# Optimization experiments

Measured on AMD Instinct MI355X. Metric: run time of the kernel, lower is better.

Reference implementation:

```python
import jax, jax.numpy as jnp
import numpy as np

N_NODES, N_EDGES, D_IN, D_HID, D_OUT = 100000, 3200000, 128, 64, 10


def _gcn_norm(src, dst, n):
    # symmetric normalization deg^{-1/2}[src] * deg^{-1/2}[dst]; edge weights = 1
    ones = jnp.ones(src.shape[0], jnp.float32)
    deg = jax.ops.segment_sum(ones, dst, num_segments=n)
    dinv = jnp.where(deg > 0, jax.lax.rsqrt(jnp.maximum(deg, 1.0)), 0.0)
    return dinv[src] * dinv[dst]


def _gcn_conv(x, W, b, src, dst, norm, n):
    h = x @ W                                   # [N, out]
    msg = norm[:, None] * jnp.take(h, src, axis=0)  # [E+N, out]
    return jax.ops.segment_sum(msg, dst, num_segments=n) + b


def setup_inputs() -> dict:
    key = jax.random.key(0)
    ks = jax.random.split(key, 8)
    x = jax.random.normal(ks[0], (N_NODES, D_IN), jnp.float32)
    edge_index = jax.random.randint(ks[1], (2, N_EDGES), 0, N_NODES, jnp.int32)
    def glorot(k, fan_in, fan_out):
        s = (6.0 / (fan_in + fan_out)) ** 0.5
        return jax.random.uniform(k, (fan_in, fan_out), jnp.float32, -s, s)
    return {
        "x": x,
        "edge_index": edge_index,
        "W1": glorot(ks[2], D_IN, D_HID), "b1": jnp.zeros((D_HID,), jnp.float32),
        "W2": glorot(ks[3], D_HID, D_HID), "b2": jnp.zeros((D_HID,), jnp.float32),
        "W3": glorot(ks[4], D_HID, D_OUT), "b3": jnp.zeros((D_OUT,), jnp.float32),
    }


def reference(x, edge_index, W1, b1, W2, b2, W3, b3):
    n = x.shape[0]
    loops = jnp.arange(n, dtype=edge_index.dtype)
    src = jnp.concatenate([edge_index[0], loops])  # add self-loops (PyG default)
    dst = jnp.concatenate([edge_index[1], loops])
    norm = _gcn_norm(src, dst, n)                  # identical for all 3 layers
    h = jax.nn.relu(_gcn_conv(x, W1, b1, src, dst, norm, n))
    h = jax.nn.relu(_gcn_conv(h, W2, b2, src, dst, norm, n))
    return _gcn_conv(h, W3, b3, src, dst, norm, n)
```

## Files before the change

### kernel.cpp

```cpp
#include <hip/hip_runtime.h>


constexpr int BK_SHIFT = 6;
constexpr int BK_NODES = 64;
constexpr int BK_CAP   = 2432;
constexpr int MAXNB    = 1568;

__device__ __forceinline__ unsigned short f2bf(float f) {
    unsigned u = __builtin_bit_cast(unsigned, f);
    u += 0x7FFF + ((u >> 16) & 1);
    return (unsigned short)(u >> 16);
}
__device__ __forceinline__ float bf_lo(unsigned d) {
    return __builtin_bit_cast(float, d << 16);
}
__device__ __forceinline__ float bf_hi(unsigned d) {
    return __builtin_bit_cast(float, d & 0xFFFF0000u);
}

__global__ void k_cursor_init(int* __restrict__ cursor, int nb) {
    int i = blockIdx.x * blockDim.x + threadIdx.x;
    if (i < nb) cursor[i] = i * BK_CAP;
}

__global__ void k_partition(const int* __restrict__ src, const int* __restrict__ dst,
                            int E, int nb, int* __restrict__ cursor,
                            unsigned* __restrict__ inter) {
    __shared__ int lcount[MAXNB];
    __shared__ int gbase[MAXNB];
    int t = threadIdx.x;
    int base = blockIdx.x * 16384;
    for (int i = t; i < MAXNB; i += 512) lcount[i] = 0;
    __syncthreads();
    int sv[32], dvv[32];
#pragma unroll
    for (int j = 0; j < 32; j++) {
        int idx = base + j * 512 + t;
        if (idx < E) {
            sv[j] = src[idx]; dvv[j] = dst[idx];
            atomicAdd(&lcount[dvv[j] >> BK_SHIFT], 1);
        } else dvv[j] = -1;
    }
    __syncthreads();
    for (int i = t; i < nb; i += 512) {
        int c = lcount[i]; int g = 0;
        if (c) g = atomicAdd(&cursor[i], c);
        gbase[i] = g; lcount[i] = 0;
    }
    __syncthreads();
#pragma unroll
    for (int j = 0; j < 32; j++) {
        if (dvv[j] >= 0) {
            int b = dvv[j] >> BK_SHIFT;
            int r = atomicAdd(&lcount[b], 1);
            int pos = gbase[b] + r;
            if (pos < (b + 1) * BK_CAP)
                inter[pos] = (unsigned)sv[j] | ((unsigned)(dvv[j] & (BK_NODES - 1)) << 20);
        }
    }
}

__global__ void k_dinvb(const unsigned* __restrict__ inter, const int* __restrict__ cursor,
                        float* __restrict__ dinv, int N) {
    __shared__ int hist[BK_NODES];
    int t = threadIdx.x, b = blockIdx.x;
    if (t < BK_NODES) hist[t] = 0;
    __syncthreads();
    int start = b * BK_CAP;
    int cnt = min(cursor[b] - start, BK_CAP);
    for (int i = t; i < cnt; i += 256) atomicAdd(&hist[inter[start + i] >> 20], 1);
    __syncthreads();
    if (t < BK_NODES) {
        int d = b * BK_NODES + t;
        if (d < N) dinv[d] = rsqrtf((float)(hist[t] + 1));
    }
}

template <int K>
__global__ void k_gemm64bf(const float* __restrict__ X, const float* __restrict__ W,
                           const float* __restrict__ dinv,
                           unsigned short* __restrict__ Y, int n) {
    __shared__ float ws[K * 64];
    __shared__ float xs[16 * K];
    int t = threadIdx.x;
    for (int i = t; i < K * 64; i += 256) ws[i] = W[i];
    int nb = blockIdx.x * 16;
    for (int i = t; i < 16 * K; i += 256) {
        int r = i / K, c = i % K;
        int node = nb + r;
        xs[i] = (node < n) ? X[(size_t)node * K + c] : 0.f;
    }
    __syncthreads();
    int node = t >> 4;
    int ch0  = (t & 15) * 4;
    float ax = 0.f, ay = 0.f, az = 0.f, aw = 0.f;
    for (int k = 0; k < K; k++) {
        float xv = xs[node * K + k];
        const float4 w = *reinterpret_cast<const float4*>(&ws[k * 64 + ch0]);
        ax += xv * w.x; ay += xv * w.y; az += xv * w.z; aw += xv * w.w;
    }
    int gn = nb + node;
    if (gn < n) {
        float dvv = dinv[gn];
        ushort4 r;
        r.x = f2bf(dvv * ax); r.y = f2bf(dvv * ay);
        r.z = f2bf(dvv * az); r.w = f2bf(dvv * aw);
        *reinterpret_cast<ushort4*>(Y + (size_t)gn * 64 + ch0) = r;
    }
}

__global__ void k_gemm10(const float* __restrict__ X, const float* __restrict__ W,
                         const float* __restrict__ dinv, float* __restrict__ Y, int n) {
    __shared__ float ws[64 * 10];
    __shared__ float xs[16 * 64];
    int t = threadIdx.x;
    for (int i = t; i < 640; i += 256) ws[i] = W[i];
    int nb = blockIdx.x * 16;
    for (int i = t; i < 16 * 64; i += 256) {
        int r = i >> 6, c = i & 63;
        int node = nb + r;
        xs[i] = (node < n) ? X[(size_t)node * 64 + c] : 0.f;
    }
    __syncthreads();
    int ns = t >> 4, c = t & 15;
    if (c < 10) {
        float acc = 0.f;
        for (int k = 0; k < 64; k++) acc += xs[ns * 64 + k] * ws[k * 10 + c];
        int node = nb + ns;
        if (node < n) Y[(size_t)node * 10 + c] = dinv[node] * acc;
    }
}

__global__ __launch_bounds__(512) void k_agg64(const unsigned short* __restrict__ H,
                        const unsigned* __restrict__ inter, const int* __restrict__ cursor,
                        const float* __restrict__ bias, float* __restrict__ out,
                        int N, int relu) {
    __shared__ unsigned raw[BK_CAP];
    __shared__ unsigned srt[BK_CAP];
    __shared__ int hist[BK_NODES];
    __shared__ int offs[BK_NODES + 1];
    __shared__ int cur[BK_NODES];
    int t = threadIdx.x, b = blockIdx.x;
    if (t < BK_NODES) hist[t] = 0;
    __syncthreads();
    int start = b * BK_CAP;
    int cnt = min(cursor[b] - start, BK_CAP);
    for (int i = t; i < cnt; i += 512) {
        unsigned r = inter[start + i];
        raw[i] = r;
        atomicAdd(&hist[r >> 20], 1);
    }
    __syncthreads();
    if (t < BK_NODES) {
        int v = hist[t];
        int inc = v;
#pragma unroll
        for (int d = 1; d < 64; d <<= 1) {
            int o = __shfl_up(inc, d);
            if (t >= d) inc += o;
        }
        offs[t + 1] = inc;
        if (t == 0) offs[0] = 0;
        cur[t] = inc - v;
    }
    __syncthreads();
    for (int i = t; i < cnt; i += 512) {
        unsigned r = raw[i];
        int pos = atomicAdd(&cur[r >> 20], 1);
        srt[pos] = r & 0xFFFFFu;
    }
    __syncthreads();
    int wv = t >> 6, lane = t & 63;
    int esub = lane >> 3, cg = lane & 7;
    for (int nd = wv; nd < BK_NODES; nd += 8) {
        int d = b * BK_NODES + nd;
        if (d >= N) break;
        int o0 = offs[nd], o1 = offs[nd + 1];
        float a0 = 0.f, a1 = 0.f, a2 = 0.f, a3 = 0.f;
        float a4 = 0.f, a5 = 0.f, a6 = 0.f, a7 = 0.f;
        int e = o0 + esub;
        for (; e + 8 < o1; e += 16) {
            int s0 = srt[e], s1 = srt[e + 8];
            const uint4 v0 = *reinterpret_cast<const uint4*>(H + ((size_t)s0 << 6) + (cg << 3));
            const uint4 v1 = *reinterpret_cast<const uint4*>(H + ((size_t)s1 << 6) + (cg << 3));
            a0 += bf_lo(v0.x); a1 += bf_hi(v0.x); a2 += bf_lo(v0.y); a3 += bf_hi(v0.y);
            a4 += bf_lo(v0.z); a5 += bf_hi(v0.z); a6 += bf_lo(v0.w); a7 += bf_hi(v0.w);
            a0 += bf_lo(v1.x); a1 += bf_hi(v1.x); a2 += bf_lo(v1.y); a3 += bf_hi(v1.y);
            a4 += bf_lo(v1.z); a5 += bf_hi(v1.z); a6 += bf_lo(v1.w); a7 += bf_hi(v1.w);
        }
        if (e < o1) {
            int s0 = srt[e];
            const uint4 v0 = *reinterpret_cast<const uint4*>(H + ((size_t)s0 << 6) + (cg << 3));
            a0 += bf_lo(v0.x); a1 += bf_hi(v0.x); a2 += bf_lo(v0.y); a3 += bf_hi(v0.y);
            a4 += bf_lo(v0.z); a5 += bf_hi(v0.z); a6 += bf_lo(v0.w); a7 += bf_hi(v0.w);
        }
#pragma unroll
        for (int m = 8; m <= 32; m <<= 1) {
            a0 += __shfl_xor(a0, m); a1 += __shfl_xor(a1, m);
            a2 += __shfl_xor(a2, m); a3 += __shfl_xor(a3, m);
            a4 += __shfl_xor(a4, m); a5 += __shfl_xor(a5, m);
            a6 += __shfl_xor(a6, m); a7 += __shfl_xor(a7, m);
        }
        if (esub == 0) {
            float dv = rsqrtf((float)(hist[nd] + 1));
            const uint4 sv = *reinterpret_cast<const uint4*>(H + ((size_t)d << 6) + (cg << 3));
            float s[8] = {bf_lo(sv.x), bf_hi(sv.x), bf_lo(sv.y), bf_hi(sv.y),
                          bf_lo(sv.z), bf_hi(sv.z), bf_lo(sv.w), bf_hi(sv.w)};
            float acc[8] = {a0, a1, a2, a3, a4, a5, a6, a7};
            const float* bp = bias + cg * 8;
            float o[8];
#pragma unroll
            for (int j = 0; j < 8; j++) {
                float val = dv * (acc[j] + s[j]) + bp[j];
                if (relu) val = fmaxf(val, 0.f);
                o[j] = val;
            }
            float4 r0 = {o[0], o[1], o[2], o[3]}, r1 = {o[4], o[5], o[6], o[7]};
            float* op = out + (size_t)d * 64 + cg * 8;
            *reinterpret_cast<float4*>(op)     = r0;
            *reinterpret_cast<float4*>(op + 4) = r1;
        }
    }
}

__global__ __launch_bounds__(512) void k_agg10(const float* __restrict__ H,
                        const unsigned* __restrict__ inter, const int* __restrict__ cursor,
                        const float* __restrict__ b3, float* __restrict__ out, int N) {
    __shared__ unsigned raw[BK_CAP];
    __shared__ unsigned srt[BK_CAP];
    __shared__ int hist[BK_NODES];
    __shared__ int offs[BK_NODES + 1];
    __shared__ int cur[BK_NODES];
    int t = threadIdx.x, b = blockIdx.x;
    if (t < BK_NODES) hist[t] = 0;
    __syncthreads();
    int start = b * BK_CAP;
    int cnt = min(cursor[b] - start, BK_CAP);
    for (int i = t; i < cnt; i += 512) {
        unsigned r = inter[start + i];
        raw[i] = r;
        atomicAdd(&hist[r >> 20], 1);
    }
    __syncthreads();
    if (t < BK_NODES) {
        int v = hist[t];
        int inc = v;
#pragma unroll
        for (int d = 1; d < 64; d <<= 1) {
            int o = __shfl_up(inc, d);
            if (t >= d) inc += o;
        }
        offs[t + 1] = inc;
        if (t == 0) offs[0] = 0;
        cur[t] = inc - v;
    }
    __syncthreads();
    for (int i = t; i < cnt; i += 512) {
        unsigned r = raw[i];
        int pos = atomicAdd(&cur[r >> 20], 1);
        srt[pos] = r & 0xFFFFFu;
    }
    __syncthreads();
    int wv = t >> 6, lane = t & 63;
    int esub = lane >> 4, c = lane & 15;
    for (int nd = wv; nd < BK_NODES; nd += 8) {
        int d = b * BK_NODES + nd;
        if (d >= N) break;
        int o0 = offs[nd], o1 = offs[nd + 1];
        float acc = 0.f;
        if (c < 10) {
            int e = o0 + esub;
            for (; e + 4 < o1; e += 8) {
                int s0 = srt[e], s1 = srt[e + 4];
                acc += H[(size_t)s0 * 10 + c] + H[(size_t)s1 * 10 + c];
            }
            if (e < o1) acc += H[(size_t)srt[e] * 10 + c];
        }
        acc += __shfl_xor(acc, 16);
        acc += __shfl_xor(acc, 32);
        if (esub == 0 && c < 10) {
            float dv = rsqrtf((float)(hist[nd] + 1));
            out[(size_t)d * 10 + c] = dv * (acc + H[(size_t)d * 10 + c]) + b3[c];
        }
    }
}

extern "C" void kernel_launch(void* const* d_in, const int* in_sizes, int n_in,
                              void* d_out, int out_size, void* d_ws, size_t ws_size,
                              hipStream_t stream) {
    const float* x  = (const float*)d_in[0];
    const int*   ei = (const int*)d_in[1];
    const float* W1 = (const float*)d_in[2];
    const float* b1 = (const float*)d_in[3];
    const float* W2 = (const float*)d_in[4];
    const float* b2 = (const float*)d_in[5];
    const float* W3 = (const float*)d_in[6];
    const float* b3 = (const float*)d_in[7];

    int N = in_sizes[0] / 128;
    int E = in_sizes[1] / 2;
    const int* esrc = ei;
    const int* edst = ei + E;
    int nb = (N + BK_NODES - 1) >> BK_SHIFT;

    char* p = (char*)d_ws;
    auto carve = [&](size_t bytes) -> void* {
        void* r = p;
        p += (bytes + 255) & ~(size_t)255;
        return r;
    };
    int*      cursor = (int*)carve((size_t)MAXNB * 4);
    unsigned* inter  = (unsigned*)carve((size_t)nb * BK_CAP * 4);
    float*    dinv   = (float*)carve((size_t)N * 4);
    unsigned short* Hs = (unsigned short*)carve((size_t)N * 64 * 2);
    float*    G      = (float*)carve((size_t)N * 64 * 4);
    float*    Hs10   = (float*)carve((size_t)N * 10 * 4);
    (void)ws_size; (void)n_in; (void)out_size;

    k_cursor_init<<<(nb + 255) / 256, 256, 0, stream>>>(cursor, nb);
    k_partition<<<(E + 16383) / 16384, 512, 0, stream>>>(esrc, edst, E, nb, cursor, inter);
    k_dinvb<<<nb, 256, 0, stream>>>(inter, cursor, dinv, N);

    k_gemm64bf<128><<<(N + 15) / 16, 256, 0, stream>>>(x, W1, dinv, Hs, N);
    k_agg64<<<nb, 512, 0, stream>>>(Hs, inter, cursor, b1, G, N, 1);
    k_gemm64bf<64><<<(N + 15) / 16, 256, 0, stream>>>(G, W2, dinv, Hs, N);
    k_agg64<<<nb, 512, 0, stream>>>(Hs, inter, cursor, b2, G, N, 1);
    k_gemm10<<<(N + 15) / 16, 256, 0, stream>>>(G, W3, dinv, Hs10, N);
    k_agg10<<<nb, 512, 0, stream>>>(Hs10, inter, cursor, b3, (float*)d_out, N);
}
```

Baseline: 297.8 us.

## Use bf16 MFMA for 64-wide GEMMs, bf16 layer-1 output, deeper gather unroll

Replaces the scalar FP32 per-node GEMM for layers 1 and 2 with a 64-node tile kernel that stages X and W as bf16 in LDS and computes with mfma_f32_16x16x32_bf16. The first aggregation now writes its output as bf16, which halves the traffic it writes and the second GEMM reads. The edge gather loops in both aggregation kernels are unrolled from 2 to 4 independent loads to raise memory-level parallelism. The cost is extra bf16 rounding of the intermediate activations, plus more register pressure in the gather loops.

New measurement: 254.1 us. -14.7%, faster.

```diff
diff --git a/kernel.cpp b/kernel.cpp
--- a/kernel.cpp
+++ b/kernel.cpp
@@ -6,10 +6,16 @@
 constexpr int BK_CAP   = 2432;
 constexpr int MAXNB    = 1568;
 
+typedef __attribute__((ext_vector_type(8))) short short8_t;
+typedef __attribute__((ext_vector_type(4))) float f32x4_t;
+
 __device__ __forceinline__ unsigned short f2bf(float f) {
     unsigned u = __builtin_bit_cast(unsigned, f);
     u += 0x7FFF + ((u >> 16) & 1);
     return (unsigned short)(u >> 16);
+}
+__device__ __forceinline__ unsigned pack2(float lo, float hi) {
+    return (unsigned)f2bf(lo) | ((unsigned)f2bf(hi) << 16);
 }
 __device__ __forceinline__ float bf_lo(unsigned d) {
     return __builtin_bit_cast(float, d << 16);
@@ -76,36 +82,63 @@
     }
 }
 
-template <int K>
-__global__ void k_gemm64bf(const float* __restrict__ X, const float* __restrict__ W,
+template <int K, bool IN_F32>
+__global__ __launch_bounds__(256) void k_gemmMF(const void* __restrict__ Xv,
+                           const float* __restrict__ W,
                            const float* __restrict__ dinv,
                            unsigned short* __restrict__ Y, int n) {
-    __shared__ float ws[K * 64];
-    __shared__ float xs[16 * K];
+    constexpr int KP = K + 8;
+    __shared__ unsigned short Al[64 * KP];
+    __shared__ unsigned short Bl[64 * KP];
     int t = threadIdx.x;
-    for (int i = t; i < K * 64; i += 256) ws[i] = W[i];
-    int nb = blockIdx.x * 16;
-    for (int i = t; i < 16 * K; i += 256) {
-        int r = i / K, c = i % K;
-        int node = nb + r;
-        xs[i] = (node < n) ? X[(size_t)node * K + c] : 0.f;
-    }
-    __syncthreads();
-    int node = t >> 4;
-    int ch0  = (t & 15) * 4;
-    float ax = 0.f, ay = 0.f, az = 0.f, aw = 0.f;
-    for (int k = 0; k < K; k++) {
-        float xv = xs[node * K + k];
-        const float4 w = *reinterpret_cast<const float4*>(&ws[k * 64 + ch0]);
-        ax += xv * w.x; ay += xv * w.y; az += xv * w.z; aw += xv * w.w;
-    }
-    int gn = nb + node;
-    if (gn < n) {
-        float dvv = dinv[gn];
-        ushort4 r;
-        r.x = f2bf(dvv * ax); r.y = f2bf(dvv * ay);
-        r.z = f2bf(dvv * az); r.w = f2bf(dvv * aw);
-        *reinterpret_cast<ushort4*>(Y + (size_t)gn * 64 + ch0) = r;
+    int nb = blockIdx.x * 64;
+    if (IN_F32) {
+        const float* X = (const float*)Xv;
+        for (int i = t * 4; i < 64 * K; i += 1024) {
+            int r = i / K, c = i % K;
+            int node = nb + r;
+            float4 v = {0.f, 0.f, 0.f, 0.f};
+            if (node < n) v = *reinterpret_cast<const float4*>(X + (size_t)node * K + c);
+            uint2 pk = {pack2(v.x, v.y), pack2(v.z, v.w)};
+            *reinterpret_cast<uint2*>(&Al[r * KP + c]) = pk;
+        }
+    } else {
+        const unsigned short* X = (const unsigned short*)Xv;
+        for (int i = t * 4; i < 64 * K; i += 1024) {
+            int r = i / K, c = i % K;
+            int node = nb + r;
+            uint2 pk = {0u, 0u};
+            if (node < n) pk = *reinterpret_cast<const uint2*>(X + (size_t)node * K + c);
+            *reinterpret_cast<uint2*>(&Al[r * KP + c]) = pk;
+        }
+    }
+    {
+        int c = t & 63, kb = t >> 6;
+        for (int k = kb; k < K; k += 4)
+            Bl[c * KP + k] = f2bf(W[k * 64 + c]);
+    }
+    __syncthreads();
+    int w = t >> 6, lane = t & 63;
+    int ml = lane & 15, kg = lane >> 4;
+    f32x4_t acc[4] = {{0,0,0,0},{0,0,0,0},{0,0,0,0},{0,0,0,0}};
+    for (int ks = 0; ks < K / 32; ks++) {
+        int ko = ks * 32 + kg * 8;
+        short8_t a = *reinterpret_cast<const short8_t*>(&Al[(16 * w + ml) * KP + ko]);
+#pragma unroll
+        for (int c = 0; c < 4; c++) {
+            short8_t b = *reinterpret_cast<const short8_t*>(&Bl[(16 * c + ml) * KP + ko]);
+            acc[c] = __builtin_amdgcn_mfma_f32_16x16x32_bf16(a, b, acc[c], 0, 0, 0);
+        }
+    }
+#pragma unroll
+    for (int r = 0; r < 4; r++) {
+        int grow = nb + 16 * w + kg * 4 + r;
+        if (grow < n) {
+            float dv = dinv[grow];
+#pragma unroll
+            for (int c = 0; c < 4; c++)
+                Y[(size_t)grow * 64 + 16 * c + ml] = f2bf(dv * acc[c][r]);
+        }
     }
 }
 
@@ -131,9 +164,10 @@
     }
 }
 
+template <int OBF>
 __global__ __launch_bounds__(512) void k_agg64(const unsigned short* __restrict__ H,
                         const unsigned* __restrict__ inter, const int* __restrict__ cursor,
-                        const float* __restrict__ bias, float* __restrict__ out,
+                        const float* __restrict__ bias, void* __restrict__ outv,
                         int N, int relu) {
     __shared__ unsigned raw[BK_CAP];
     __shared__ unsigned srt[BK_CAP];
@@ -172,6 +206,7 @@
     __syncthreads();
     int wv = t >> 6, lane = t & 63;
     int esub = lane >> 3, cg = lane & 7;
+    const unsigned short* Hc = H + (cg << 3);
     for (int nd = wv; nd < BK_NODES; nd += 8) {
         int d = b * BK_NODES + nd;
         if (d >= N) break;
@@ -179,18 +214,24 @@
         float a0 = 0.f, a1 = 0.f, a2 = 0.f, a3 = 0.f;
         float a4 = 0.f, a5 = 0.f, a6 = 0.f, a7 = 0.f;
         int e = o0 + esub;
-        for (; e + 8 < o1; e += 16) {
-            int s0 = srt[e], s1 = srt[e + 8];
-            const uint4 v0 = *reinterpret_cast<const uint4*>(H + ((size_t)s0 << 6) + (cg << 3));
-            const uint4 v1 = *reinterpret_cast<const uint4*>(H + ((size_t)s1 << 6) + (cg << 3));
+        for (; e + 24 < o1; e += 32) {
+            int s0 = srt[e], s1 = srt[e + 8], s2 = srt[e + 16], s3 = srt[e + 24];
+            const uint4 v0 = *reinterpret_cast<const uint4*>(Hc + ((size_t)s0 << 6));
+            const uint4 v1 = *reinterpret_cast<const uint4*>(Hc + ((size_t)s1 << 6));
+            const uint4 v2 = *reinterpret_cast<const uint4*>(Hc + ((size_t)s2 << 6));
+            const uint4 v3 = *reinterpret_cast<const uint4*>(Hc + ((size_t)s3 << 6));
             a0 += bf_lo(v0.x); a1 += bf_hi(v0.x); a2 += bf_lo(v0.y); a3 += bf_hi(v0.y);
             a4 += bf_lo(v0.z); a5 += bf_hi(v0.z); a6 += bf_lo(v0.w); a7 += bf_hi(v0.w);
             a0 += bf_lo(v1.x); a1 += bf_hi(v1.x); a2 += bf_lo(v1.y); a3 += bf_hi(v1.y);
             a4 += bf_lo(v1.z); a5 += bf_hi(v1.z); a6 += bf_lo(v1.w); a7 += bf_hi(v1.w);
-        }
-        if (e < o1) {
+            a0 += bf_lo(v2.x); a1 += bf_hi(v2.x); a2 += bf_lo(v2.y); a3 += bf_hi(v2.y);
+            a4 += bf_lo(v2.z); a5 += bf_hi(v2.z); a6 += bf_lo(v2.w); a7 += bf_hi(v2.w);
+            a0 += bf_lo(v3.x); a1 += bf_hi(v3.x); a2 += bf_lo(v3.y); a3 += bf_hi(v3.y);
+            a4 += bf_lo(v3.z); a5 += bf_hi(v3.z); a6 += bf_lo(v3.w); a7 += bf_hi(v3.w);
+        }
+        for (; e < o1; e += 8) {
             int s0 = srt[e];
-            const uint4 v0 = *reinterpret_cast<const uint4*>(H + ((size_t)s0 << 6) + (cg << 3));
+            const uint4 v0 = *reinterpret_cast<const uint4*>(Hc + ((size_t)s0 << 6));
             a0 += bf_lo(v0.x); a1 += bf_hi(v0.x); a2 += bf_lo(v0.y); a3 += bf_hi(v0.y);
             a4 += bf_lo(v0.z); a5 += bf_hi(v0.z); a6 += bf_lo(v0.w); a7 += bf_hi(v0.w);
         }
@@ -203,7 +244,7 @@
         }
         if (esub == 0) {
             float dv = rsqrtf((float)(hist[nd] + 1));
-            const uint4 sv = *reinterpret_cast<const uint4*>(H + ((size_t)d << 6) + (cg << 3));
+            const uint4 sv = *reinterpret_cast<const uint4*>(Hc + ((size_t)d << 6));
             float s[8] = {bf_lo(sv.x), bf_hi(sv.x), bf_lo(sv.y), bf_hi(sv.y),
                           bf_lo(sv.z), bf_hi(sv.z), bf_lo(sv.w), bf_hi(sv.w)};
             float acc[8] = {a0, a1, a2, a3, a4, a5, a6, a7};
@@ -215,10 +256,17 @@
                 if (relu) val = fmaxf(val, 0.f);
                 o[j] = val;
             }
-            float4 r0 = {o[0], o[1], o[2], o[3]}, r1 = {o[4], o[5], o[6], o[7]};
-            float* op = out + (size_t)d * 64 + cg * 8;
-            *reinterpret_cast<float4*>(op)     = r0;
-            *reinterpret_cast<float4*>(op + 4) = r1;
+            if (OBF) {
+                unsigned short* op = (unsigned short*)outv + (size_t)d * 64 + cg * 8;
+                uint4 pk = {pack2(o[0], o[1]), pack2(o[2], o[3]),
+                            pack2(o[4], o[5]), pack2(o[6], o[7])};
+                *reinterpret_cast<uint4*>(op) = pk;
+            } else {
+                float* op = (float*)outv + (size_t)d * 64 + cg * 8;
+                float4 r0 = {o[0], o[1], o[2], o[3]}, r1 = {o[4], o[5], o[6], o[7]};
+                *reinterpret_cast<float4*>(op)     = r0;
+                *reinterpret_cast<float4*>(op + 4) = r1;
+            }
         }
     }
 }
@@ -270,11 +318,13 @@
         float acc = 0.f;
         if (c < 10) {
             int e = o0 + esub;
-            for (; e + 4 < o1; e += 8) {
-                int s0 = srt[e], s1 = srt[e + 4];
-                acc += H[(size_t)s0 * 10 + c] + H[(size_t)s1 * 10 + c];
+            for (; e + 12 < o1; e += 16) {
+                int s0 = srt[e], s1 = srt[e + 4], s2 = srt[e + 8], s3 = srt[e + 12];
+                float h0 = H[(size_t)s0 * 10 + c], h1 = H[(size_t)s1 * 10 + c];
+                float h2 = H[(size_t)s2 * 10 + c], h3 = H[(size_t)s3 * 10 + c];
+                acc += (h0 + h1) + (h2 + h3);
             }
-            if (e < o1) acc += H[(size_t)srt[e] * 10 + c];
+            for (; e < o1; e += 4) acc += H[(size_t)srt[e] * 10 + c];
         }
         acc += __shfl_xor(acc, 16);
         acc += __shfl_xor(acc, 32);
@@ -313,7 +363,8 @@
     unsigned* inter  = (unsigned*)carve((size_t)nb * BK_CAP * 4);
     float*    dinv   = (float*)carve((size_t)N * 4);
     unsigned short* Hs = (unsigned short*)carve((size_t)N * 64 * 2);
-    float*    G      = (float*)carve((size_t)N * 64 * 4);
+    unsigned short* Gb = (unsigned short*)carve((size_t)N * 64 * 2);
+    float*    Gf     = (float*)carve((size_t)N * 64 * 4);
     float*    Hs10   = (float*)carve((size_t)N * 10 * 4);
     (void)ws_size; (void)n_in; (void)out_size;
 
@@ -321,10 +372,10 @@
     k_partition<<<(E + 16383) / 16384, 512, 0, stream>>>(esrc, edst, E, nb, cursor, inter);
     k_dinvb<<<nb, 256, 0, stream>>>(inter, cursor, dinv, N);
 
-    k_gemm64bf<128><<<(N + 15) / 16, 256, 0, stream>>>(x, W1, dinv, Hs, N);
-    k_agg64<<<nb, 512, 0, stream>>>(Hs, inter, cursor, b1, G, N, 1);
-    k_gemm64bf<64><<<(N + 15) / 16, 256, 0, stream>>>(G, W2, dinv, Hs, N);
-    k_agg64<<<nb, 512, 0, stream>>>(Hs, inter, cursor, b2, G, N, 1);
-    k_gemm10<<<(N + 15) / 16, 256, 0, stream>>>(G, W3, dinv, Hs10, N);
+    k_gemmMF<128, true><<<(N + 63) / 64, 256, 0, stream>>>(x, W1, dinv, Hs, N);
+    k_agg64<1><<<nb, 512, 0, stream>>>(Hs, inter, cursor, b1, Gb, N, 1);
+    k_gemmMF<64, false><<<(N + 63) / 64, 256, 0, stream>>>(Gb, W2, dinv, Hs, N);
+    k_agg64<0><<<nb, 512, 0, stream>>>(Hs, inter, cursor, b2, Gf, N, 1);
+    k_gemm10<<<(N + 15) / 16, 256, 0, stream>>>(Gf, W3, dinv, Hs10, N);
     k_agg10<<<nb, 512, 0, stream>>>(Hs10, inter, cursor, b3, (float*)d_out, N);
 }
```
